# Performance work log

Hardware: AMD Instinct MI355X
Metric: run time of the kernel (lower is better)

The kernel has to match this reference:

```python
import jax, jax.numpy as jnp
import numpy as np

LEAKY = 0.2  # tf.nn.leaky_relu default alpha
E_SZ = [64, 64, 16]
F_SZ = [128, 128, 8]
N_MAPS, C, H, W = 64, 1, 32, 32
B = 8192


def _leaky(x):
    return jnp.where(x >= 0, x, LEAKY * x)


def func_theta(x, theta, sz, in_sz):
    # x: [B, in_sz]; theta: [B, total]; per-sample MLP with weights sliced from theta
    y = x
    offset = 0
    n = len(sz)
    for i, out_sz in enumerate(sz):
        w_sz = in_sz * out_sz
        Wm = theta[:, offset:offset + w_sz].reshape(-1, in_sz, out_sz)
        offset += w_sz
        b = theta[:, offset:offset + out_sz]
        offset += out_sz
        y = jnp.einsum('bi,bio->bo', y, Wm) + b
        if i < n - 1:
            y = _leaky(y)
        in_sz = out_sz
    return y


def setup_inputs() -> dict:
    key = jax.random.key(0)
    ks = jax.random.split(key, 16)

    def g(k, shape, scale):
        return (jax.random.normal(k, shape, dtype=jnp.float32) * scale)

    inp = {
        'indices': jax.random.randint(ks[0], (B,), 0, N_MAPS, dtype=jnp.int32),
        'states': jax.random.normal(ks[1], (B, 4), dtype=jnp.float32),
        'maps': jax.random.normal(ks[2], (N_MAPS, C, H, W), dtype=jnp.float32),
        'fc1_w': g(ks[3], (C * H * W, 256), 1.0 / np.sqrt(C * H * W)),
        'fc1_b': jnp.zeros((256,), jnp.float32),
        'fc2_w': g(ks[4], (256, 128), 1.0 / np.sqrt(256)),
        'fc2_b': jnp.zeros((128,), jnp.float32),
        'fc3_w': g(ks[5], (128, 128), 1.0 / np.sqrt(128)),
        'fc3_b': jnp.zeros((128,), jnp.float32),
        'bn_w': g(ks[6], (128, 32), 1.0 / np.sqrt(128)),
        'bn_b': jnp.zeros((32,), jnp.float32),
        'e_w': g(ks[7], (32, 5456), 1e-5),
        'e_b': g(ks[8], (5456,), 1e-3),
        'f_w': g(ks[9], (32, 21768), 1e-5),
        'f_b': g(ks[10], (21768,), 1e-3),
    }
    return inp


def reference(indices, states, maps, fc1_w, fc1_b, fc2_w, fc2_b, fc3_w, fc3_b,
              bn_w, bn_b, e_w, e_b, f_w, f_b):
    # gather maps per sample and flatten (NCHW -> NHWC transpose is a no-op after flatten
    # mathematically, but keep the exact data layout of the original)
    m = jnp.transpose(maps[indices], (0, 2, 3, 1)).astype(jnp.float32)  # [B,H,W,C]
    z = m.reshape(m.shape[0], -1)

    # hypernet trunk
    z = _leaky(z @ fc1_w + fc1_b)
    z = _leaky(z @ fc2_w + fc2_b)
    z = _leaky(z @ fc3_w + fc3_b)
    z = z @ bn_w + bn_b  # bottleneck, no activation
    theta_e = z @ e_w + e_b  # [B, 5456]
    theta_f = z @ f_w + f_b  # [B, 21768]

    S = states[:, 0:2]
    G = states[:, 2:4]
    e_s = func_theta(S, theta_e, E_SZ, 2)
    e_g = func_theta(G, theta_e, E_SZ, 2)
    zf = jnp.concatenate([e_s, e_g], axis=-1)  # [B, 32]
    ang = func_theta(zf, theta_f, F_SZ, 2 * E_SZ[-1])  # [B, 8]
    pts = jnp.concatenate([jnp.sin(ang), jnp.cos(ang)], axis=-1)  # [B, 16]
    return pts
```

## Files before the change

### kernel.cpp

```cpp
#include <hip/hip_runtime.h>
#include <hip/hip_bf16.h>


#define LEAKY 0.2f
#define NCLS 64
#define B_TOT 8192
#define NSLICE 3


__device__ __forceinline__ float lrelu(float x) { return x >= 0.f ? x : LEAKY * x; }

__global__ __launch_bounds__(1024) void fc1_kernel(
    const float* __restrict__ maps, const float* __restrict__ fc1_w,
    const float* __restrict__ fc1_b, float* __restrict__ h1g)
{
    __shared__ float m[1024];
    __shared__ float red[1024];
    const int t = threadIdx.x;
    const int c = blockIdx.x >> 2;
    const int q = blockIdx.x & 3;

    m[t] = maps[(size_t)c * 1024 + t];
    __syncthreads();

    const int ol = t & 63, ks = t >> 6;
    const int o = q * 64 + ol;
    const float* wp = fc1_w + o;
    float acc = 0.f;
#pragma unroll 8
    for (int i = 0; i < 64; ++i) {
        const int k = ks * 64 + i;
        acc += m[k] * wp[(size_t)k * 256];
    }
    red[t] = acc;
    __syncthreads();
    if (t < 64) {
        float a = fc1_b[q * 64 + t];
#pragma unroll
        for (int r = 0; r < 16; ++r) a += red[r * 64 + t];
        h1g[c * 256 + q * 64 + t] = lrelu(a);
    }
}

__global__ __launch_bounds__(1024) void backbone_bucket_kernel(
    const float* __restrict__ h1g,
    const float* __restrict__ fc2_w, const float* __restrict__ fc2_b,
    const float* __restrict__ fc3_w, const float* __restrict__ fc3_b,
    const float* __restrict__ bn_w,  const float* __restrict__ bn_b,
    float* __restrict__ z,
    const int* __restrict__ idx, int* __restrict__ counts,
    int* __restrict__ offsets, int* __restrict__ perm)
{
    __shared__ float red[1024];
    __shared__ float h1[256];
    __shared__ float h2[128];
    __shared__ float h3[128];
    __shared__ int cnt[16][64];
    __shared__ int wcur[16][64];

    const int t = threadIdx.x;

    if (blockIdx.x == 64) {
        const int w = t >> 6;
        cnt[w][t & 63] = 0;
        __syncthreads();
        int my[8];
#pragma unroll
        for (int r = 0; r < 8; ++r) {
            my[r] = idx[r * 1024 + t];
            atomicAdd(&cnt[w][my[r]], 1);
        }
        __syncthreads();
        if (t < 64) {
            int run = 0;
#pragma unroll
            for (int w2 = 0; w2 < 16; ++w2) {
                const int v = cnt[w2][t];
                wcur[w2][t] = run;
                run += v;
            }
            counts[t] = run;
            int x = run;
            for (int d = 1; d < 64; d <<= 1) {
                const int y = __shfl_up(x, d, 64);
                if (t >= d) x += y;
            }
            const int basec = x - run;
            offsets[t] = basec;
#pragma unroll
            for (int w2 = 0; w2 < 16; ++w2) wcur[w2][t] += basec;
        }
        __syncthreads();
#pragma unroll
        for (int r = 0; r < 8; ++r) {
            const int p = atomicAdd(&wcur[w][my[r]], 1);
            perm[p] = r * 1024 + t;
        }
        return;
    }

    const int c = blockIdx.x;
    if (t < 256) h1[t] = h1g[c * 256 + t];
    __syncthreads();

    {
        const int o = t & 127, ks = t >> 7;
        float acc = 0.f;
#pragma unroll
        for (int i = 0; i < 32; ++i) {
            const int k = ks * 32 + i;
            acc += h1[k] * fc2_w[k * 128 + o];
        }
        red[t] = acc;
    }
    __syncthreads();
    if (t < 128) {
        float a = fc2_b[t];
#pragma unroll
        for (int r = 0; r < 8; ++r) a += red[r * 128 + t];
        h2[t] = lrelu(a);
    }
    __syncthreads();
    {
        const int o = t & 127, ks = t >> 7;
        float acc = 0.f;
#pragma unroll
        for (int i = 0; i < 16; ++i) {
            const int k = ks * 16 + i;
            acc += h2[k] * fc3_w[k * 128 + o];
        }
        red[t] = acc;
    }
    __syncthreads();
    if (t < 128) {
        float a = fc3_b[t];
#pragma unroll
        for (int r = 0; r < 8; ++r) a += red[r * 128 + t];
        h3[t] = lrelu(a);
    }
    __syncthreads();
    {
        const int o = t & 31, ks = t >> 5;
        float acc = 0.f;
#pragma unroll
        for (int i = 0; i < 4; ++i) {
            const int k = ks * 4 + i;
            acc += h3[k] * bn_w[k * 32 + o];
        }
        red[t] = acc;
    }
    __syncthreads();
    if (t < 32) {
        float a = bn_b[t];
#pragma unroll
        for (int r = 0; r < 32; ++r) a += red[r * 32 + t];
        z[c * 32 + t] = a;
    }
}

__global__ __launch_bounds__(256) void theta_kernel(
    const float* __restrict__ z,
    const float* __restrict__ e_w, const float* __restrict__ e_b,
    const float* __restrict__ f_w, const float* __restrict__ f_b,
    float* __restrict__ th_e, float* __restrict__ th_f)
{
    __shared__ __align__(16) float zl[2048];
    const int t = threadIdx.x;
    ((float4*)zl)[t]       = ((const float4*)z)[t];
    ((float4*)zl)[t + 256] = ((const float4*)z)[t + 256];
    __syncthreads();

    int j = blockIdx.x * 256 + t;
    const int cbase = blockIdx.y * 8;
    const float* wbase;
    float* op;
    int stride;
    float bias;
    if (j < 5456) {
        wbase = e_w + j; bias = e_b[j]; op = th_e + j; stride = 5456;
    } else {
        const int jj = j - 5456;
        if (jj >= 21768) return;
        wbase = f_w + jj; bias = f_b[jj]; op = th_f + jj; stride = 21768;
    }
    float wk[32];
#pragma unroll
    for (int k = 0; k < 32; ++k) wk[k] = wbase[(size_t)k * stride];

#pragma unroll
    for (int cc = 0; cc < 8; cc += 4) {
        const int c0 = cbase + cc;
        float a0 = bias, a1 = bias, a2 = bias, a3 = bias;
#pragma unroll
        for (int k4 = 0; k4 < 8; ++k4) {
            const float4 z0 = *(const float4*)&zl[(c0 + 0) * 32 + k4 * 4];
            const float4 z1 = *(const float4*)&zl[(c0 + 1) * 32 + k4 * 4];
            const float4 z2 = *(const float4*)&zl[(c0 + 2) * 32 + k4 * 4];
            const float4 z3 = *(const float4*)&zl[(c0 + 3) * 32 + k4 * 4];
            const float w0 = wk[k4 * 4], w1 = wk[k4 * 4 + 1];
            const float w2 = wk[k4 * 4 + 2], w3 = wk[k4 * 4 + 3];
            a0 += z0.x * w0 + z0.y * w1 + z0.z * w2 + z0.w * w3;
            a1 += z1.x * w0 + z1.y * w1 + z1.z * w2 + z1.w * w3;
            a2 += z2.x * w0 + z2.y * w1 + z2.z * w2 + z2.w * w3;
            a3 += z3.x * w0 + z3.y * w1 + z3.z * w2 + z3.w * w3;
        }
        op[(size_t)(c0 + 0) * stride] = a0;
        op[(size_t)(c0 + 1) * stride] = a1;
        op[(size_t)(c0 + 2) * stride] = a2;
        op[(size_t)(c0 + 3) * stride] = a3;
    }
}

#define ESTRIDE 68
#define FSTRIDE 132

#define K3_LDS_FLOATS 36376
#define K3_LDS_BYTES  (K3_LDS_FLOATS * 4)

__global__ __launch_bounds__(512) void func_kernel(
    const float* __restrict__ states,
    const float* __restrict__ th_e_all, const float* __restrict__ th_f_all,
    const int* __restrict__ counts, const int* __restrict__ offsets,
    const int* __restrict__ perm, float* __restrict__ out)
{
    extern __shared__ float smem[];
    float* wE   = smem;
    float* wFa  = smem + 5392;
    float* wH   = smem + 10776;
    float* actA = smem + 18968;
    float* actB = smem + 27672;

    const int c = blockIdx.x;
    const int s = blockIdx.y;
    const int nb   = counts[c];
    const int base = offsets[c];
    const int nblk = (nb + 63) >> 6;
    const int npass = (nblk > s) ? ((nblk - 1 - s) / NSLICE + 1) : 0;
    if (npass == 0) return;

    const float* te = th_e_all + (size_t)c * 5456;
    const float* tf = th_f_all + (size_t)c * 21768;

    const int t  = threadIdx.x;
    const int b  = t & 31;
    const int v  = t & 63;
    const int ge = t >> 6;
    const int gf = t >> 5;
    const int cole = ge * 8;
    const int colf = gf * 8;
    const int eoffL = v * ESTRIDE;
    const int eoffH = (v + 64) * ESTRIDE;
    const int foff0 = b * FSTRIDE;
    const int foff1 = (b + 32) * FSTRIDE;

    for (int j = t * 4; j < 5392; j += 2048)
        *(float4*)&wE[j] = *(const float4*)&te[j];
    for (int j = t * 4; j < 4224; j += 2048)
        *(float4*)&wFa[j] = *(const float4*)&tf[j];
    for (int j = t * 4; j < 1160; j += 2048)
        *(float4*)&wFa[4224 + j] = *(const float4*)&tf[20608 + j];

    for (int p = 0; p < npass; ++p) {
        __syncthreads();

        for (int j = t * 4; j < 8192; j += 2048)
            *(float4*)&wH[j] = *(const float4*)&tf[4224 + j];

        const int kbase = (p * NSLICE + s) << 6;
        const int ib_e  = kbase + v;
        const int bi_e  = (ib_e < nb) ? perm[base + ib_e] : 0;
        const float4 st = *(const float4*)&states[(size_t)bi_e * 4];

        {
            const float4 wa0 = *(const float4*)&wE[cole];
            const float4 wa1 = *(const float4*)&wE[cole + 4];
            const float4 wb0 = *(const float4*)&wE[64 + cole];
            const float4 wb1 = *(const float4*)&wE[64 + cole + 4];
            const float4 bb0 = *(const float4*)&wE[128 + cole];
            const float4 bb1 = *(const float4*)&wE[128 + cole + 4];
            float4 o0, o1;
            o0.x = lrelu(st.x * wa0.x + st.y * wb0.x + bb0.x);
            o0.y = lrelu(st.x * wa0.y + st.y * wb0.y + bb0.y);
            o0.z = lrelu(st.x * wa0.z + st.y * wb0.z + bb0.z);
            o0.w = lrelu(st.x * wa0.w + st.y * wb0.w + bb0.w);
            o1.x = lrelu(st.x * wa1.x + st.y * wb1.x + bb1.x);
            o1.y = lrelu(st.x * wa1.y + st.y * wb1.y + bb1.y);
            o1.z = lrelu(st.x * wa1.z + st.y * wb1.z + bb1.z);
            o1.w = lrelu(st.x * wa1.w + st.y * wb1.w + bb1.w);
            *(float4*)&actA[eoffL + cole]     = o0;
            *(float4*)&actA[eoffL + cole + 4] = o1;
            o0.x = lrelu(st.z * wa0.x + st.w * wb0.x + bb0.x);
            o0.y = lrelu(st.z * wa0.y + st.w * wb0.y + bb0.y);
            o0.z = lrelu(st.z * wa0.z + st.w * wb0.z + bb0.z);
            o0.w = lrelu(st.z * wa0.w + st.w * wb0.w + bb0.w);
            o1.x = lrelu(st.z * wa1.x + st.w * wb1.x + bb1.x);
            o1.y = lrelu(st.z * wa1.y + st.w * wb1.y + bb1.y);
            o1.z = lrelu(st.z * wa1.z + st.w * wb1.z + bb1.z);
            o1.w = lrelu(st.z * wa1.w + st.w * wb1.w + bb1.w);
            *(float4*)&actA[eoffH + cole]     = o0;
            *(float4*)&actA[eoffH + cole + 4] = o1;
        }
        __syncthreads();

        {
            float aL[8] = {0,0,0,0,0,0,0,0};
            float aH[8] = {0,0,0,0,0,0,0,0};
#pragma unroll 4
            for (int i4 = 0; i4 < 16; ++i4) {
                const float4 yL = *(const float4*)&actA[eoffL + i4 * 4];
                const float4 yH = *(const float4*)&actA[eoffH + i4 * 4];
#pragma unroll
                for (int u = 0; u < 4; ++u) {
                    const int row = 192 + (i4 * 4 + u) * 64 + cole;
                    const float4 wA = *(const float4*)&wE[row];
                    const float4 wB = *(const float4*)&wE[row + 4];
                    const float yl = (&yL.x)[u], yh = (&yH.x)[u];
                    aL[0] += yl * wA.x; aL[1] += yl * wA.y;
                    aL[2] += yl * wA.z; aL[3] += yl * wA.w;
                    aL[4] += yl * wB.x; aL[5] += yl * wB.y;
                    aL[6] += yl * wB.z; aL[7] += yl * wB.w;
                    aH[0] += yh * wA.x; aH[1] += yh * wA.y;
                    aH[2] += yh * wA.z; aH[3] += yh * wA.w;
                    aH[4] += yh * wB.x; aH[5] += yh * wB.y;
                    aH[6] += yh * wB.z; aH[7] += yh * wB.w;
                }
            }
            const float4 bA = *(const float4*)&wE[4288 + cole];
            const float4 bB = *(const float4*)&wE[4288 + cole + 4];
            float4 o0, o1;
            o0.x = lrelu(aL[0] + bA.x); o0.y = lrelu(aL[1] + bA.y);
            o0.z = lrelu(aL[2] + bA.z); o0.w = lrelu(aL[3] + bA.w);
            o1.x = lrelu(aL[4] + bB.x); o1.y = lrelu(aL[5] + bB.y);
            o1.z = lrelu(aL[6] + bB.z); o1.w = lrelu(aL[7] + bB.w);
            *(float4*)&actB[eoffL + cole]     = o0;
            *(float4*)&actB[eoffL + cole + 4] = o1;
            o0.x = lrelu(aH[0] + bA.x); o0.y = lrelu(aH[1] + bA.y);
            o0.z = lrelu(aH[2] + bA.z); o0.w = lrelu(aH[3] + bA.w);
            o1.x = lrelu(aH[4] + bB.x); o1.y = lrelu(aH[5] + bB.y);
            o1.z = lrelu(aH[6] + bB.z); o1.w = lrelu(aH[7] + bB.w);
            *(float4*)&actB[eoffH + cole]     = o0;
            *(float4*)&actB[eoffH + cole + 4] = o1;
        }
        __syncthreads();

        {
            const int col3 = ge * 2;
            float a0 = 0.f, a1 = 0.f, a2 = 0.f, a3 = 0.f;
#pragma unroll 4
            for (int i4 = 0; i4 < 16; ++i4) {
                const float4 yL = *(const float4*)&actB[eoffL + i4 * 4];
                const float4 yH = *(const float4*)&actB[eoffH + i4 * 4];
#pragma unroll
                for (int u = 0; u < 4; ++u) {
                    const float2 w2 = *(const float2*)&wE[4352 + (i4 * 4 + u) * 16 + col3];
                    const float yl = (&yL.x)[u], yh = (&yH.x)[u];
                    a0 += yl * w2.x; a1 += yl * w2.y;
                    a2 += yh * w2.x; a3 += yh * w2.y;
                }
            }
            const float b0 = wE[5376 + col3], b1 = wE[5376 + col3 + 1];
            actA[v * FSTRIDE + col3]          = a0 + b0;
            actA[v * FSTRIDE + col3 + 1]      = a1 + b1;
            actA[v * FSTRIDE + 16 + col3]     = a2 + b0;
            actA[v * FSTRIDE + 16 + col3 + 1] = a3 + b1;
        }
        __syncthreads();

        {
            float a0[8] = {0,0,0,0,0,0,0,0};
            float a1[8] = {0,0,0,0,0,0,0,0};
#pragma unroll
            for (int i4 = 0; i4 < 8; ++i4) {
                const float4 y0 = *(const float4*)&actA[foff0 + i4 * 4];
                const float4 y1 = *(const float4*)&actA[foff1 + i4 * 4];
#pragma unroll
                for (int u = 0; u < 4; ++u) {
                    const int row = (i4 * 4 + u) * 128 + colf;
                    const float4 wA = *(const float4*)&wFa[row];
                    const float4 wB = *(const float4*)&wFa[row + 4];
                    const float ya = (&y0.x)[u], yb = (&y1.x)[u];
                    a0[0] += ya * wA.x; a0[1] += ya * wA.y;
                    a0[2] += ya * wA.z; a0[3] += ya * wA.w;
                    a0[4] += ya * wB.x; a0[5] += ya * wB.y;
                    a0[6] += ya * wB.z; a0[7] += ya * wB.w;
                    a1[0] += yb * wA.x; a1[1] += yb * wA.y;
                    a1[2] += yb * wA.z; a1[3] += yb * wA.w;
                    a1[4] += yb * wB.x; a1[5] += yb * wB.y;
                    a1[6] += yb * wB.z; a1[7] += yb * wB.w;
                }
            }
            const float4 bA = *(const float4*)&wFa[4096 + colf];
            const float4 bB = *(const float4*)&wFa[4096 + colf + 4];
            float4 o0, o1;
            o0.x = lrelu(a0[0] + bA.x); o0.y = lrelu(a0[1] + bA.y);
            o0.z = lrelu(a0[2] + bA.z); o0.w = lrelu(a0[3] + bA.w);
            o1.x = lrelu(a0[4] + bB.x); o1.y = lrelu(a0[5] + bB.y);
            o1.z = lrelu(a0[6] + bB.z); o1.w = lrelu(a0[7] + bB.w);
            *(float4*)&actB[foff0 + colf]     = o0;
            *(float4*)&actB[foff0 + colf + 4] = o1;
            o0.x = lrelu(a1[0] + bA.x); o0.y = lrelu(a1[1] + bA.y);
            o0.z = lrelu(a1[2] + bA.z); o0.w = lrelu(a1[3] + bA.w);
            o1.x = lrelu(a1[4] + bB.x); o1.y = lrelu(a1[5] + bB.y);
            o1.z = lrelu(a1[6] + bB.z); o1.w = lrelu(a1[7] + bB.w);
            *(float4*)&actB[foff1 + colf]     = o0;
            *(float4*)&actB[foff1 + colf + 4] = o1;
        }
        __syncthreads();

        {
            float a0[8] = {0,0,0,0,0,0,0,0};
            float a1[8] = {0,0,0,0,0,0,0,0};
#pragma unroll 4
            for (int i4 = 0; i4 < 16; ++i4) {
                const float4 y0 = *(const float4*)&actB[foff0 + i4 * 4];
                const float4 y1 = *(const float4*)&actB[foff1 + i4 * 4];
#pragma unroll
                for (int u = 0; u < 4; ++u) {
                    const int row = (i4 * 4 + u) * 128 + colf;
                    const float4 wA = *(const float4*)&wH[row];
                    const float4 wB = *(const float4*)&wH[row + 4];
                    const float ya = (&y0.x)[u], yb = (&y1.x)[u];
                    a0[0] += ya * wA.x; a0[1] += ya * wA.y;
                    a0[2] += ya * wA.z; a0[3] += ya * wA.w;
                    a0[4] += ya * wB.x; a0[5] += ya * wB.y;
                    a0[6] += ya * wB.z; a0[7] += ya * wB.w;
                    a1[0] += yb * wA.x; a1[1] += yb * wA.y;
                    a1[2] += yb * wA.z; a1[3] += yb * wA.w;
                    a1[4] += yb * wB.x; a1[5] += yb * wB.y;
                    a1[6] += yb * wB.z; a1[7] += yb * wB.w;
                }
            }
            __syncthreads();
            for (int j = t * 4; j < 8192; j += 2048)
                *(float4*)&wH[j] = *(const float4*)&tf[4224 + 8192 + j];
            __syncthreads();
#pragma unroll 4
            for (int i4 = 0; i4 < 16; ++i4) {
                const float4 y0 = *(const float4*)&actB[foff0 + 64 + i4 * 4];
                const float4 y1 = *(const float4*)&actB[foff1 + 64 + i4 * 4];
#pragma unroll
                for (int u = 0; u < 4; ++u) {
                    const int row = (i4 * 4 + u) * 128 + colf;
                    const float4 wA = *(const float4*)&wH[row];
                    const float4 wB = *(const float4*)&wH[row + 4];
                    const float ya = (&y0.x)[u], yb = (&y1.x)[u];
                    a0[0] += ya * wA.x; a0[1] += ya * wA.y;
                    a0[2] += ya * wA.z; a0[3] += ya * wA.w;
                    a0[4] += ya * wB.x; a0[5] += ya * wB.y;
                    a0[6] += ya * wB.z; a0[7] += ya * wB.w;
                    a1[0] += yb * wA.x; a1[1] += yb * wA.y;
                    a1[2] += yb * wA.z; a1[3] += yb * wA.w;
                    a1[4] += yb * wB.x; a1[5] += yb * wB.y;
                    a1[6] += yb * wB.z; a1[7] += yb * wB.w;
                }
            }
            const float4 bA = *(const float4*)&wFa[4224 + colf];
            const float4 bB = *(const float4*)&wFa[4224 + colf + 4];
            float4 o0, o1;
            o0.x = lrelu(a0[0] + bA.x); o0.y = lrelu(a0[1] + bA.y);
            o0.z = lrelu(a0[2] + bA.z); o0.w = lrelu(a0[3] + bA.w);
            o1.x = lrelu(a0[4] + bB.x); o1.y = lrelu(a0[5] + bB.y);
            o1.z = lrelu(a0[6] + bB.z); o1.w = lrelu(a0[7] + bB.w);
            *(float4*)&actA[foff0 + colf]     = o0;
            *(float4*)&actA[foff0 + colf + 4] = o1;
            o0.x = lrelu(a1[0] + bA.x); o0.y = lrelu(a1[1] + bA.y);
            o0.z = lrelu(a1[2] + bA.z); o0.w = lrelu(a1[3] + bA.w);
            o1.x = lrelu(a1[4] + bB.x); o1.y = lrelu(a1[5] + bB.y);
            o1.z = lrelu(a1[6] + bB.z); o1.w = lrelu(a1[7] + bB.w);
            *(float4*)&actA[foff1 + colf]     = o0;
            *(float4*)&actA[foff1 + colf + 4] = o1;
        }
        __syncthreads();

        if (gf < 8) {
            float a0 = 0.f, a1 = 0.f;
#pragma unroll 8
            for (int i4 = 0; i4 < 32; ++i4) {
                const float4 y0 = *(const float4*)&actA[foff0 + i4 * 4];
                const float4 y1 = *(const float4*)&actA[foff1 + i4 * 4];
#pragma unroll
                for (int u = 0; u < 4; ++u) {
                    const float w = wFa[4352 + (i4 * 4 + u) * 8 + gf];
                    a0 += (&y0.x)[u] * w;
                    a1 += (&y1.x)[u] * w;
                }
            }
            const float bb = wFa[5376 + gf];
            a0 += bb; a1 += bb;
            const int ib0 = kbase + b, ib1 = kbase + b + 32;
            if (ib0 < nb) {
                const int bi = perm[base + ib0];
                out[(size_t)bi * 16 + gf]     = __sinf(a0);
                out[(size_t)bi * 16 + 8 + gf] = __cosf(a0);
            }
            if (ib1 < nb) {
                const int bi = perm[base + ib1];
                out[(size_t)bi * 16 + gf]     = __sinf(a1);
                out[(size_t)bi * 16 + 8 + gf] = __cosf(a1);
            }
        }
    }
}

extern "C" void kernel_launch(void* const* d_in, const int* in_sizes, int n_in,
                              void* d_out, int out_size, void* d_ws, size_t ws_size,
                              hipStream_t stream)
{
    const int*   indices = (const int*)  d_in[0];
    const float* states  = (const float*)d_in[1];
    const float* maps    = (const float*)d_in[2];
    const float* fc1_w   = (const float*)d_in[3];
    const float* fc1_b   = (const float*)d_in[4];
    const float* fc2_w   = (const float*)d_in[5];
    const float* fc2_b   = (const float*)d_in[6];
    const float* fc3_w   = (const float*)d_in[7];
    const float* fc3_b   = (const float*)d_in[8];
    const float* bn_w    = (const float*)d_in[9];
    const float* bn_b    = (const float*)d_in[10];
    const float* e_w     = (const float*)d_in[11];
    const float* e_b     = (const float*)d_in[12];
    const float* f_w     = (const float*)d_in[13];
    const float* f_b     = (const float*)d_in[14];
    float* out = (float*)d_out;

    float* ws   = (float*)d_ws;
    float* z    = ws;
    float* th_e = ws + 2048;
    float* th_f = ws + 351232;
    int* counts  = (int*)(ws + 1744384);
    int* offsets = counts + 64;
    int* perm    = counts + 128;
    float* h1g   = ws + 1752704;

    static int s_lds_optin = 0;
    if (!s_lds_optin) {
        hipFuncSetAttribute((const void*)func_kernel,
                            hipFuncAttributeMaxDynamicSharedMemorySize,
                            K3_LDS_BYTES);
        s_lds_optin = 1;
    }

    fc1_kernel<<<256, 1024, 0, stream>>>(maps, fc1_w, fc1_b, h1g);
    backbone_bucket_kernel<<<65, 1024, 0, stream>>>(
        h1g, fc2_w, fc2_b, fc3_w, fc3_b, bn_w, bn_b, z,
        indices, counts, offsets, perm);
    theta_kernel<<<dim3(107, 8), 256, 0, stream>>>(
        z, e_w, e_b, f_w, f_b, th_e, th_f);
    func_kernel<<<dim3(NCLS, NSLICE), 512, K3_LDS_BYTES, stream>>>(
        states, th_e, th_f, counts, offsets, perm, out);
}
```

Before: 130.7 us.

## Split each class evenly across four slices with 48-sample passes

The per-class work split in func_kernel changes. Before, the kernel used three slices that took 64-sample blocks round-robin. Now it uses four slices, each owning a contiguous range of about nb/4 samples, processed in passes of up to 48 samples. The aim is to balance load across blocks, reduce padding waste in the last pass, and cut the LDS footprint so more blocks fit per CU. The trade-off is that only 256 of the 512 threads do the matmul stages (3 rows each), leaving half the block idle for most of the pass, and the θ_f hidden weights are reloaded once per pass per block.

```diff
diff --git a/kernel.cpp b/kernel.cpp
--- a/kernel.cpp
+++ b/kernel.cpp
@@ -5,7 +5,7 @@
 #define LEAKY 0.2f
 #define NCLS 64
 #define B_TOT 8192
-#define NSLICE 3
+#define CAP 48
 
 
 __device__ __forceinline__ float lrelu(float x) { return x >= 0.f ? x : LEAKY * x; }
@@ -214,7 +214,7 @@
 #define ESTRIDE 68
 #define FSTRIDE 132
 
-#define K3_LDS_FLOATS 36376
+#define K3_LDS_FLOATS 32024
 #define K3_LDS_BYTES  (K3_LDS_FLOATS * 4)
 
 __global__ __launch_bounds__(512) void func_kernel(
@@ -228,30 +228,27 @@
     float* wFa  = smem + 5392;
     float* wH   = smem + 10776;
     float* actA = smem + 18968;
-    float* actB = smem + 27672;
+    float* actB = smem + 25496;
 
     const int c = blockIdx.x;
     const int s = blockIdx.y;
     const int nb   = counts[c];
     const int base = offsets[c];
-    const int nblk = (nb + 63) >> 6;
-    const int npass = (nblk > s) ? ((nblk - 1 - s) / NSLICE + 1) : 0;
-    if (npass == 0) return;
+    const int q = nb >> 2, r = nb & 3;
+    const int lo  = s * q + (s < r ? s : r);
+    const int cnt = q + (s < r ? 1 : 0);
+    if (cnt == 0) return;
+    const int hi = lo + cnt;
 
     const float* te = th_e_all + (size_t)c * 5456;
     const float* tf = th_f_all + (size_t)c * 21768;
 
     const int t  = threadIdx.x;
-    const int b  = t & 31;
-    const int v  = t & 63;
-    const int ge = t >> 6;
-    const int gf = t >> 5;
-    const int cole = ge * 8;
-    const int colf = gf * 8;
-    const int eoffL = v * ESTRIDE;
-    const int eoffH = (v + 64) * ESTRIDE;
-    const int foff0 = b * FSTRIDE;
-    const int foff1 = (b + 32) * FSTRIDE;
+    const int eg = t & 7,  vp = t >> 3;
+    const int bp = t & 15, fg = t >> 4;
+    const int cole = eg * 8;
+    const int colf = fg * 8;
+    const int col8 = t & 7, fb3 = t >> 3;
 
     for (int j = t * 4; j < 5392; j += 2048)
         *(float4*)&wE[j] = *(const float4*)&te[j];
@@ -260,133 +257,169 @@
     for (int j = t * 4; j < 1160; j += 2048)
         *(float4*)&wFa[4224 + j] = *(const float4*)&tf[20608 + j];
 
+    const int npass = (cnt + CAP - 1) / CAP;
     for (int p = 0; p < npass; ++p) {
         __syncthreads();
 
         for (int j = t * 4; j < 8192; j += 2048)
             *(float4*)&wH[j] = *(const float4*)&tf[4224 + j];
 
-        const int kbase = (p * NSLICE + s) << 6;
-        const int ib_e  = kbase + v;
-        const int bi_e  = (ib_e < nb) ? perm[base + ib_e] : 0;
-        const float4 st = *(const float4*)&states[(size_t)bi_e * 4];
-
-        {
+        const int pb = lo + p * CAP;
+
+        if (t < 256) {
             const float4 wa0 = *(const float4*)&wE[cole];
             const float4 wa1 = *(const float4*)&wE[cole + 4];
             const float4 wb0 = *(const float4*)&wE[64 + cole];
             const float4 wb1 = *(const float4*)&wE[64 + cole + 4];
             const float4 bb0 = *(const float4*)&wE[128 + cole];
             const float4 bb1 = *(const float4*)&wE[128 + cole + 4];
-            float4 o0, o1;
-            o0.x = lrelu(st.x * wa0.x + st.y * wb0.x + bb0.x);
-            o0.y = lrelu(st.x * wa0.y + st.y * wb0.y + bb0.y);
-            o0.z = lrelu(st.x * wa0.z + st.y * wb0.z + bb0.z);
-            o0.w = lrelu(st.x * wa0.w + st.y * wb0.w + bb0.w);
-            o1.x = lrelu(st.x * wa1.x + st.y * wb1.x + bb1.x);
-            o1.y = lrelu(st.x * wa1.y + st.y * wb1.y + bb1.y);
-            o1.z = lrelu(st.x * wa1.z + st.y * wb1.z + bb1.z);
-            o1.w = lrelu(st.x * wa1.w + st.y * wb1.w + bb1.w);
-            *(float4*)&actA[eoffL + cole]     = o0;
-            *(float4*)&actA[eoffL + cole + 4] = o1;
-            o0.x = lrelu(st.z * wa0.x + st.w * wb0.x + bb0.x);
-            o0.y = lrelu(st.z * wa0.y + st.w * wb0.y + bb0.y);
-            o0.z = lrelu(st.z * wa0.z + st.w * wb0.z + bb0.z);
-            o0.w = lrelu(st.z * wa0.w + st.w * wb0.w + bb0.w);
-            o1.x = lrelu(st.z * wa1.x + st.w * wb1.x + bb1.x);
-            o1.y = lrelu(st.z * wa1.y + st.w * wb1.y + bb1.y);
-            o1.z = lrelu(st.z * wa1.z + st.w * wb1.z + bb1.z);
-            o1.w = lrelu(st.z * wa1.w + st.w * wb1.w + bb1.w);
-            *(float4*)&actA[eoffH + cole]     = o0;
-            *(float4*)&actA[eoffH + cole + 4] = o1;
-        }
-        __syncthreads();
-
-        {
-            float aL[8] = {0,0,0,0,0,0,0,0};
-            float aH[8] = {0,0,0,0,0,0,0,0};
+#pragma unroll
+            for (int sub = 0; sub < 3; ++sub) {
+                const int vb = vp + 32 * sub;
+                const int fb = vb >> 1, ve = vb & 1;
+                const int ib = pb + fb;
+                const int bi = (ib < hi) ? perm[base + ib] : 0;
+                const float2 sv = *(const float2*)&states[(size_t)bi * 4 + 2 * ve];
+                float4 o0, o1;
+                o0.x = lrelu(sv.x * wa0.x + sv.y * wb0.x + bb0.x);
+                o0.y = lrelu(sv.x * wa0.y + sv.y * wb0.y + bb0.y);
+                o0.z = lrelu(sv.x * wa0.z + sv.y * wb0.z + bb0.z);
+                o0.w = lrelu(sv.x * wa0.w + sv.y * wb0.w + bb0.w);
+                o1.x = lrelu(sv.x * wa1.x + sv.y * wb1.x + bb1.x);
+                o1.y = lrelu(sv.x * wa1.y + sv.y * wb1.y + bb1.y);
+                o1.z = lrelu(sv.x * wa1.z + sv.y * wb1.z + bb1.z);
+                o1.w = lrelu(sv.x * wa1.w + sv.y * wb1.w + bb1.w);
+                *(float4*)&actA[vb * ESTRIDE + cole]     = o0;
+                *(float4*)&actA[vb * ESTRIDE + cole + 4] = o1;
+            }
+        }
+        __syncthreads();
+
+        if (t < 256) {
+            const int e0 = vp * ESTRIDE;
+            const int e1 = (vp + 32) * ESTRIDE;
+            const int e2 = (vp + 64) * ESTRIDE;
+            float a0[8] = {0,0,0,0,0,0,0,0};
+            float a1[8] = {0,0,0,0,0,0,0,0};
+            float a2[8] = {0,0,0,0,0,0,0,0};
 #pragma unroll 4
             for (int i4 = 0; i4 < 16; ++i4) {
-                const float4 yL = *(const float4*)&actA[eoffL + i4 * 4];
-                const float4 yH = *(const float4*)&actA[eoffH + i4 * 4];
+                const float4 y0 = *(const float4*)&actA[e0 + i4 * 4];
+                const float4 y1 = *(const float4*)&actA[e1 + i4 * 4];
+                const float4 y2 = *(const float4*)&actA[e2 + i4 * 4];
 #pragma unroll
                 for (int u = 0; u < 4; ++u) {
                     const int row = 192 + (i4 * 4 + u) * 64 + cole;
                     const float4 wA = *(const float4*)&wE[row];
                     const float4 wB = *(const float4*)&wE[row + 4];
-                    const float yl = (&yL.x)[u], yh = (&yH.x)[u];
-                    aL[0] += yl * wA.x; aL[1] += yl * wA.y;
-                    aL[2] += yl * wA.z; aL[3] += yl * wA.w;
-                    aL[4] += yl * wB.x; aL[5] += yl * wB.y;
-                    aL[6] += yl * wB.z; aL[7] += yl * wB.w;
-                    aH[0] += yh * wA.x; aH[1] += yh * wA.y;
-                    aH[2] += yh * wA.z; aH[3] += yh * wA.w;
-                    aH[4] += yh * wB.x; aH[5] += yh * wB.y;
-                    aH[6] += yh * wB.z; aH[7] += yh * wB.w;
+                    const float v0 = (&y0.x)[u], v1 = (&y1.x)[u], v2 = (&y2.x)[u];
+                    a0[0] += v0 * wA.x; a0[1] += v0 * wA.y;
+                    a0[2] += v0 * wA.z; a0[3] += v0 * wA.w;
+                    a0[4] += v0 * wB.x; a0[5] += v0 * wB.y;
+                    a0[6] += v0 * wB.z; a0[7] += v0 * wB.w;
+                    a1[0] += v1 * wA.x; a1[1] += v1 * wA.y;
+                    a1[2] += v1 * wA.z; a1[3] += v1 * wA.w;
+                    a1[4] += v1 * wB.x; a1[5] += v1 * wB.y;
+                    a1[6] += v1 * wB.z; a1[7] += v1 * wB.w;
+                    a2[0] += v2 * wA.x; a2[1] += v2 * wA.y;
+                    a2[2] += v2 * wA.z; a2[3] += v2 * wA.w;
+                    a2[4] += v2 * wB.x; a2[5] += v2 * wB.y;
+                    a2[6] += v2 * wB.z; a2[7] += v2 * wB.w;
                 }
             }
             const float4 bA = *(const float4*)&wE[4288 + cole];
             const float4 bB = *(const float4*)&wE[4288 + cole + 4];
             float4 o0, o1;
-            o0.x = lrelu(aL[0] + bA.x); o0.y = lrelu(aL[1] + bA.y);
-            o0.z = lrelu(aL[2] + bA.z); o0.w = lrelu(aL[3] + bA.w);
-            o1.x = lrelu(aL[4] + bB.x); o1.y = lrelu(aL[5] + bB.y);
-            o1.z = lrelu(aL[6] + bB.z); o1.w = lrelu(aL[7] + bB.w);
-            *(float4*)&actB[eoffL + cole]     = o0;
-            *(float4*)&actB[eoffL + cole + 4] = o1;
-            o0.x = lrelu(aH[0] + bA.x); o0.y = lrelu(aH[1] + bA.y);
-            o0.z = lrelu(aH[2] + bA.z); o0.w = lrelu(aH[3] + bA.w);
-            o1.x = lrelu(aH[4] + bB.x); o1.y = lrelu(aH[5] + bB.y);
-            o1.z = lrelu(aH[6] + bB.z); o1.w = lrelu(aH[7] + bB.w);
-            *(float4*)&actB[eoffH + cole]     = o0;
-            *(float4*)&actB[eoffH + cole + 4] = o1;
-        }
-        __syncthreads();
-
-        {
-            const int col3 = ge * 2;
-            float a0 = 0.f, a1 = 0.f, a2 = 0.f, a3 = 0.f;
+            o0.x = lrelu(a0[0] + bA.x); o0.y = lrelu(a0[1] + bA.y);
+            o0.z = lrelu(a0[2] + bA.z); o0.w = lrelu(a0[3] + bA.w);
+            o1.x = lrelu(a0[4] + bB.x); o1.y = lrelu(a0[5] + bB.y);
+            o1.z = lrelu(a0[6] + bB.z); o1.w = lrelu(a0[7] + bB.w);
+            *(float4*)&actB[e0 + cole]     = o0;
+            *(float4*)&actB[e0 + cole + 4] = o1;
+            o0.x = lrelu(a1[0] + bA.x); o0.y = lrelu(a1[1] + bA.y);
+            o0.z = lrelu(a1[2] + bA.z); o0.w = lrelu(a1[3] + bA.w);
+            o1.x = lrelu(a1[4] + bB.x); o1.y = lrelu(a1[5] + bB.y);
+            o1.z = lrelu(a1[6] + bB.z); o1.w = lrelu(a1[7] + bB.w);
+            *(float4*)&actB[e1 + cole]     = o0;
+            *(float4*)&actB[e1 + cole + 4] = o1;
+            o0.x = lrelu(a2[0] + bA.x); o0.y = lrelu(a2[1] + bA.y);
+            o0.z = lrelu(a2[2] + bA.z); o0.w = lrelu(a2[3] + bA.w);
+            o1.x = lrelu(a2[4] + bB.x); o1.y = lrelu(a2[5] + bB.y);
+            o1.z = lrelu(a2[6] + bB.z); o1.w = lrelu(a2[7] + bB.w);
+            *(float4*)&actB[e2 + cole]     = o0;
+            *(float4*)&actB[e2 + cole + 4] = o1;
+        }
+        __syncthreads();
+
+        if (t < 256) {
+            const int col3 = eg * 2;
+            const int e0 = vp * ESTRIDE;
+            const int e1 = (vp + 32) * ESTRIDE;
+            const int e2 = (vp + 64) * ESTRIDE;
+            float a00 = 0.f, a01 = 0.f, a10 = 0.f, a11 = 0.f, a20 = 0.f, a21 = 0.f;
 #pragma unroll 4
             for (int i4 = 0; i4 < 16; ++i4) {
-                const float4 yL = *(const float4*)&actB[eoffL + i4 * 4];
-                const float4 yH = *(const float4*)&actB[eoffH + i4 * 4];
+                const float4 y0 = *(const float4*)&actB[e0 + i4 * 4];
+                const float4 y1 = *(const float4*)&actB[e1 + i4 * 4];
+                const float4 y2 = *(const float4*)&actB[e2 + i4 * 4];
 #pragma unroll
                 for (int u = 0; u < 4; ++u) {
                     const float2 w2 = *(const float2*)&wE[4352 + (i4 * 4 + u) * 16 + col3];
-                    const float yl = (&yL.x)[u], yh = (&yH.x)[u];
-                    a0 += yl * w2.x; a1 += yl * w2.y;
-                    a2 += yh * w2.x; a3 += yh * w2.y;
+                    const float v0 = (&y0.x)[u], v1 = (&y1.x)[u], v2 = (&y2.x)[u];
+                    a00 += v0 * w2.x; a01 += v0 * w2.y;
+                    a10 += v1 * w2.x; a11 += v1 * w2.y;
+                    a20 += v2 * w2.x; a21 += v2 * w2.y;
                 }
             }
             const float b0 = wE[5376 + col3], b1 = wE[5376 + col3 + 1];
-            actA[v * FSTRIDE + col3]          = a0 + b0;
-            actA[v * FSTRIDE + col3 + 1]      = a1 + b1;
-            actA[v * FSTRIDE + 16 + col3]     = a2 + b0;
-            actA[v * FSTRIDE + 16 + col3 + 1] = a3 + b1;
-        }
-        __syncthreads();
-
-        {
+            {
+                const int vb = vp, fb = vb >> 1, ve = vb & 1;
+                actA[fb * FSTRIDE + ve * 16 + col3]     = a00 + b0;
+                actA[fb * FSTRIDE + ve * 16 + col3 + 1] = a01 + b1;
+            }
+            {
+                const int vb = vp + 32, fb = vb >> 1, ve = vb & 1;
+                actA[fb * FSTRIDE + ve * 16 + col3]     = a10 + b0;
+                actA[fb * FSTRIDE + ve * 16 + col3 + 1] = a11 + b1;
+            }
+            {
+                const int vb = vp + 64, fb = vb >> 1, ve = vb & 1;
+                actA[fb * FSTRIDE + ve * 16 + col3]     = a20 + b0;
+                actA[fb * FSTRIDE + ve * 16 + col3 + 1] = a21 + b1;
+            }
+        }
+        __syncthreads();
+
+        if (t < 256) {
+            const int f0 = bp * FSTRIDE;
+            const int f1 = (bp + 16) * FSTRIDE;
+            const int f2 = (bp + 32) * FSTRIDE;
             float a0[8] = {0,0,0,0,0,0,0,0};
             float a1[8] = {0,0,0,0,0,0,0,0};
+            float a2[8] = {0,0,0,0,0,0,0,0};
 #pragma unroll
             for (int i4 = 0; i4 < 8; ++i4) {
-                const float4 y0 = *(const float4*)&actA[foff0 + i4 * 4];
-                const float4 y1 = *(const float4*)&actA[foff1 + i4 * 4];
+                const float4 y0 = *(const float4*)&actA[f0 + i4 * 4];
+                const float4 y1 = *(const float4*)&actA[f1 + i4 * 4];
+                const float4 y2 = *(const float4*)&actA[f2 + i4 * 4];
 #pragma unroll
                 for (int u = 0; u < 4; ++u) {
                     const int row = (i4 * 4 + u) * 128 + colf;
                     const float4 wA = *(const float4*)&wFa[row];
                     const float4 wB = *(const float4*)&wFa[row + 4];
-                    const float ya = (&y0.x)[u], yb = (&y1.x)[u];
-                    a0[0] += ya * wA.x; a0[1] += ya * wA.y;
-                    a0[2] += ya * wA.z; a0[3] += ya * wA.w;
-                    a0[4] += ya * wB.x; a0[5] += ya * wB.y;
-                    a0[6] += ya * wB.z; a0[7] += ya * wB.w;
-                    a1[0] += yb * wA.x; a1[1] += yb * wA.y;
-                    a1[2] += yb * wA.z; a1[3] += yb * wA.w;
-                    a1[4] += yb * wB.x; a1[5] += yb * wB.y;
-                    a1[6] += yb * wB.z; a1[7] += yb * wB.w;
+                    const float v0 = (&y0.x)[u], v1 = (&y1.x)[u], v2 = (&y2.x)[u];
+                    a0[0] += v0 * wA.x; a0[1] += v0 * wA.y;
+                    a0[2] += v0 * wA.z; a0[3] += v0 * wA.w;
+                    a0[4] += v0 * wB.x; a0[5] += v0 * wB.y;
+                    a0[6] += v0 * wB.z; a0[7] += v0 * wB.w;
+                    a1[0] += v1 * wA.x; a1[1] += v1 * wA.y;
+                    a1[2] += v1 * wA.z; a1[3] += v1 * wA.w;
+                    a1[4] += v1 * wB.x; a1[5] += v1 * wB.y;
+                    a1[6] += v1 * wB.z; a1[7] += v1 * wB.w;
+                    a2[0] += v2 * wA.x; a2[1] += v2 * wA.y;
+                    a2[2] += v2 * wA.z; a2[3] += v2 * wA.w;
+                    a2[4] += v2 * wB.x; a2[5] += v2 * wB.y;
+                    a2[6] += v2 * wB.z; a2[7] += v2 * wB.w;
                 }
             }
             const float4 bA = *(const float4*)&wFa[4096 + colf];
@@ -396,107 +429,128 @@
             o0.z = lrelu(a0[2] + bA.z); o0.w = lrelu(a0[3] + bA.w);
             o1.x = lrelu(a0[4] + bB.x); o1.y = lrelu(a0[5] + bB.y);
             o1.z = lrelu(a0[6] + bB.z); o1.w = lrelu(a0[7] + bB.w);
-            *(float4*)&actB[foff0 + colf]     = o0;
-            *(float4*)&actB[foff0 + colf + 4] = o1;
+            *(float4*)&actB[f0 + colf]     = o0;
+            *(float4*)&actB[f0 + colf + 4] = o1;
             o0.x = lrelu(a1[0] + bA.x); o0.y = lrelu(a1[1] + bA.y);
             o0.z = lrelu(a1[2] + bA.z); o0.w = lrelu(a1[3] + bA.w);
             o1.x = lrelu(a1[4] + bB.x); o1.y = lrelu(a1[5] + bB.y);
             o1.z = lrelu(a1[6] + bB.z); o1.w = lrelu(a1[7] + bB.w);
-            *(float4*)&actB[foff1 + colf]     = o0;
-            *(float4*)&actB[foff1 + colf + 4] = o1;
+            *(float4*)&actB[f1 + colf]     = o0;
+            *(float4*)&actB[f1 + colf + 4] = o1;
+            o0.x = lrelu(a2[0] + bA.x); o0.y = lrelu(a2[1] + bA.y);
+            o0.z = lrelu(a2[2] + bA.z); o0.w = lrelu(a2[3] + bA.w);
+            o1.x = lrelu(a2[4] + bB.x); o1.y = lrelu(a2[5] + bB.y);
+            o1.z = lrelu(a2[6] + bB.z); o1.w = lrelu(a2[7] + bB.w);
+            *(float4*)&actB[f2 + colf]     = o0;
+            *(float4*)&actB[f2 + colf + 4] = o1;
         }
         __syncthreads();
 
         {
+            const int f0 = bp * FSTRIDE;
+            const int f1 = (bp + 16) * FSTRIDE;
+            const int f2 = (bp + 32) * FSTRIDE;
             float a0[8] = {0,0,0,0,0,0,0,0};
             float a1[8] = {0,0,0,0,0,0,0,0};
+            float a2[8] = {0,0,0,0,0,0,0,0};
+            if (t < 256) {
 #pragma unroll 4
-            for (int i4 = 0; i4 < 16; ++i4) {
-                const float4 y0 = *(const float4*)&actB[foff0 + i4 * 4];
-                const float4 y1 = *(const float4*)&actB[foff1 + i4 * 4];
-#pragma unroll
-                for (int u = 0; u < 4; ++u) {
-                    const int row = (i4 * 4 + u) * 128 + colf;
-                    const float4 wA = *(const float4*)&wH[row];
-                    const float4 wB = *(const float4*)&wH[row + 4];
-                    const float ya = (&y0.x)[u], yb = (&y1.x)[u];
-                    a0[0] += ya * wA.x; a0[1] += ya * wA.y;
-                    a0[2] += ya * wA.z; a0[3] += ya * wA.w;
-                    a0[4] += ya * wB.x; a0[5] += ya * wB.y;
-                    a0[6] += ya * wB.z; a0[7] += ya * wB.w;
-                    a1[0] += yb * wA.x; a1[1] += yb * wA.y;
-                    a1[2] += yb * wA.z; a1[3] += yb * wA.w;
-                    a1[4] += yb * wB.x; a1[5] += yb * wB.y;
-                    a1[6] += yb * wB.z; a1[7] += yb * wB.w;
+                for (int i4 = 0; i4 < 16; ++i4) {
+                    const float4 y0 = *(const float4*)&actB[f0 + i4 * 4];
+                    const float4 y1 = *(const float4*)&actB[f1 + i4 * 4];
+                    const float4 y2 = *(const float4*)&actB[f2 + i4 * 4];
+#pragma unroll
+                    for (int u = 0; u < 4; ++u) {
+                        const int row = (i4 * 4 + u) * 128 + colf;
+                        const float4 wA = *(const float4*)&wH[row];
+                        const float4 wB = *(const float4*)&wH[row + 4];
+                        const float v0 = (&y0.x)[u], v1 = (&y1.x)[u], v2 = (&y2.x)[u];
+                        a0[0] += v0 * wA.x; a0[1] += v0 * wA.y;
+                        a0[2] += v0 * wA.z; a0[3] += v0 * wA.w;
+                        a0[4] += v0 * wB.x; a0[5] += v0 * wB.y;
+                        a0[6] += v0 * wB.z; a0[7] += v0 * wB.w;
+                        a1[0] += v1 * wA.x; a1[1] += v1 * wA.y;
+                        a1[2] += v1 * wA.z; a1[3] += v1 * wA.w;
+                        a1[4] += v1 * wB.x; a1[5] += v1 * wB.y;
+                        a1[6] += v1 * wB.z; a1[7] += v1 * wB.w;
+                        a2[0] += v2 * wA.x; a2[1] += v2 * wA.y;
+                        a2[2] += v2 * wA.z; a2[3] += v2 * wA.w;
+                        a2[4] += v2 * wB.x; a2[5] += v2 * wB.y;
+                        a2[6] += v2 * wB.z; a2[7] += v2 * wB.w;
+                    }
                 }
             }
             __syncthreads();
             for (int j = t * 4; j < 8192; j += 2048)
                 *(float4*)&wH[j] = *(const float4*)&tf[4224 + 8192 + j];
             __syncthreads();
+            if (t < 256) {
 #pragma unroll 4
-            for (int i4 = 0; i4 < 16; ++i4) {
-                const float4 y0 = *(const float4*)&actB[foff0 + 64 + i4 * 4];
-                const float4 y1 = *(const float4*)&actB[foff1 + 64 + i4 * 4];
-#pragma unroll
-                for (int u = 0; u < 4; ++u) {
-                    const int row = (i4 * 4 + u) * 128 + colf;
-                    const float4 wA = *(const float4*)&wH[row];
-                    const float4 wB = *(const float4*)&wH[row + 4];
-                    const float ya = (&y0.x)[u], yb = (&y1.x)[u];
-                    a0[0] += ya * wA.x; a0[1] += ya * wA.y;
-                    a0[2] += ya * wA.z; a0[3] += ya * wA.w;
-                    a0[4] += ya * wB.x; a0[5] += ya * wB.y;
-                    a0[6] += ya * wB.z; a0[7] += ya * wB.w;
-                    a1[0] += yb * wA.x; a1[1] += yb * wA.y;
-                    a1[2] += yb * wA.z; a1[3] += yb * wA.w;
-                    a1[4] += yb * wB.x; a1[5] += yb * wB.y;
-                    a1[6] += yb * wB.z; a1[7] += yb * wB.w;
+                for (int i4 = 0; i4 < 16; ++i4) {
+                    const float4 y0 = *(const float4*)&actB[f0 + 64 + i4 * 4];
+                    const float4 y1 = *(const float4*)&actB[f1 + 64 + i4 * 4];
+                    const float4 y2 = *(const float4*)&actB[f2 + 64 + i4 * 4];
+#pragma unroll
+                    for (int u = 0; u < 4; ++u) {
+                        const int row = (i4 * 4 + u) * 128 + colf;
+                        const float4 wA = *(const float4*)&wH[row];
+                        const float4 wB = *(const float4*)&wH[row + 4];
+                        const float v0 = (&y0.x)[u], v1 = (&y1.x)[u], v2 = (&y2.x)[u];
+                        a0[0] += v0 * wA.x; a0[1] += v0 * wA.y;
+                        a0[2] += v0 * wA.z; a0[3] += v0 * wA.w;
+                        a0[4] += v0 * wB.x; a0[5] += v0 * wB.y;
+                        a0[6] += v0 * wB.z; a0[7] += v0 * wB.w;
+                        a1[0] += v1 * wA.x; a1[1] += v1 * wA.y;
+                        a1[2] += v1 * wA.z; a1[3] += v1 * wA.w;
+                        a1[4] += v1 * wB.x; a1[5] += v1 * wB.y;
+                        a1[6] += v1 * wB.z; a1[7] += v1 * wB.w;
+                        a2[0] += v2 * wA.x; a2[1] += v2 * wA.y;
+                        a2[2] += v2 * wA.z; a2[3] += v2 * wA.w;
+                        a2[4] += v2 * wB.x; a2[5] += v2 * wB.y;
+                        a2[6] += v2 * wB.z; a2[7] += v2 * wB.w;
+                    }
                 }
-            }
-            const float4 bA = *(const float4*)&wFa[4224 + colf];
-            const float4 bB = *(const float4*)&wFa[4224 + colf + 4];
-            float4 o0, o1;
-            o0.x = lrelu(a0[0] + bA.x); o0.y = lrelu(a0[1] + bA.y);
-            o0.z = lrelu(a0[2] + bA.z); o0.w = lrelu(a0[3] + bA.w);
-            o1.x = lrelu(a0[4] + bB.x); o1.y = lrelu(a0[5] + bB.y);
-            o1.z = lrelu(a0[6] + bB.z); o1.w = lrelu(a0[7] + bB.w);
-            *(float4*)&actA[foff0 + colf]     = o0;
-            *(float4*)&actA[foff0 + colf + 4] = o1;
-            o0.x = lrelu(a1[0] + bA.x); o0.y = lrelu(a1[1] + bA.y);
-            o0.z = lrelu(a1[2] + bA.z); o0.w = lrelu(a1[3] + bA.w);
-            o1.x = lrelu(a1[4] + bB.x); o1.y = lrelu(a1[5] + bB.y);
-            o1.z = lrelu(a1[6] + bB.z); o1.w = lrelu(a1[7] + bB.w);
-            *(float4*)&actA[foff1 + colf]     = o0;
-            *(float4*)&actA[foff1 + colf + 4] = o1;
-        }
-        __syncthreads();
-
-        if (gf < 8) {
-            float a0 = 0.f, a1 = 0.f;
+                const float4 bA = *(const float4*)&wFa[4224 + colf];
+                const float4 bB = *(const float4*)&wFa[4224 + colf + 4];
+                float4 o0, o1;
+                o0.x = lrelu(a0[0] + bA.x); o0.y = lrelu(a0[1] + bA.y);
+                o0.z = lrelu(a0[2] + bA.z); o0.w = lrelu(a0[3] + bA.w);
+                o1.x = lrelu(a0[4] + bB.x); o1.y = lrelu(a0[5] + bB.y);
+                o1.z = lrelu(a0[6] + bB.z); o1.w = lrelu(a0[7] + bB.w);
+                *(float4*)&actA[f0 + colf]     = o0;
+                *(float4*)&actA[f0 + colf + 4] = o1;
+                o0.x = lrelu(a1[0] + bA.x); o0.y = lrelu(a1[1] + bA.y);
+                o0.z = lrelu(a1[2] + bA.z); o0.w = lrelu(a1[3] + bA.w);
+                o1.x = lrelu(a1[4] + bB.x); o1.y = lrelu(a1[5] + bB.y);
+                o1.z = lrelu(a1[6] + bB.z); o1.w = lrelu(a1[7] + bB.w);
+                *(float4*)&actA[f1 + colf]     = o0;
+                *(float4*)&actA[f1 + colf + 4] = o1;
+                o0.x = lrelu(a2[0] + bA.x); o0.y = lrelu(a2[1] + bA.y);
+                o0.z = lrelu(a2[2] + bA.z); o0.w = lrelu(a2[3] + bA.w);
+                o1.x = lrelu(a2[4] + bB.x); o1.y = lrelu(a2[5] + bB.y);
+                o1.z = lrelu(a2[6] + bB.z); o1.w = lrelu(a2[7] + bB.w);
+                *(float4*)&actA[f2 + colf]     = o0;
+                *(float4*)&actA[f2 + colf + 4] = o1;
+            }
+        }
+        __syncthreads();
+
+        if (fb3 < CAP) {
+            const int ib = pb + fb3;
+            if (ib < hi) {
+                const int foff = fb3 * FSTRIDE;
+                float a = 0.f;
 #pragma unroll 8
-            for (int i4 = 0; i4 < 32; ++i4) {
-                const float4 y0 = *(const float4*)&actA[foff0 + i4 * 4];
-                const float4 y1 = *(const float4*)&actA[foff1 + i4 * 4];
-#pragma unroll
-                for (int u = 0; u < 4; ++u) {
-                    const float w = wFa[4352 + (i4 * 4 + u) * 8 + gf];
-                    a0 += (&y0.x)[u] * w;
-                    a1 += (&y1.x)[u] * w;
+                for (int i4 = 0; i4 < 32; ++i4) {
+                    const float4 y4 = *(const float4*)&actA[foff + i4 * 4];
+#pragma unroll
+                    for (int u = 0; u < 4; ++u)
+                        a += (&y4.x)[u] * wFa[4352 + (i4 * 4 + u) * 8 + col8];
                 }
-            }
-            const float bb = wFa[5376 + gf];
-            a0 += bb; a1 += bb;
-            const int ib0 = kbase + b, ib1 = kbase + b + 32;
-            if (ib0 < nb) {
-                const int bi = perm[base + ib0];
-                out[(size_t)bi * 16 + gf]     = __sinf(a0);
-                out[(size_t)bi * 16 + 8 + gf] = __cosf(a0);
-            }
-            if (ib1 < nb) {
-                const int bi = perm[base + ib1];
-                out[(size_t)bi * 16 + gf]     = __sinf(a1);
-                out[(size_t)bi * 16 + 8 + gf] = __cosf(a1);
+                a += wFa[5376 + col8];
+                const int bi = perm[base + ib];
+                out[(size_t)bi * 16 + col8]     = __sinf(a);
+                out[(size_t)bi * 16 + 8 + col8] = __cosf(a);
             }
         }
     }
@@ -546,6 +600,6 @@
         indices, counts, offsets, perm);
     theta_kernel<<<dim3(107, 8), 256, 0, stream>>>(
         z, e_w, e_b, f_w, f_b, th_e, th_f);
-    func_kernel<<<dim3(NCLS, NSLICE), 512, K3_LDS_BYTES, stream>>>(
+    func_kernel<<<dim3(NCLS, 4), 512, K3_LDS_BYTES, stream>>>(
         states, th_e, th_f, counts, offsets, perm, out);
 }
```

New measurement: 130.5 us. Within noise of the previous version (-0.2%).
